# Optimization experiments

Measured on AMD Instinct MI355X. Metric: run time of the kernel, lower is better.

## Reference

```python
import jax, jax.numpy as jnp
import numpy as np


def setup_inputs() -> dict:
    key = jax.random.key(0)
    kx, kw = jax.random.split(key)
    x = jax.random.normal(kx, (4096, 4096), dtype=jnp.float32)
    weight = jax.random.uniform(kw, (7, 7), dtype=jnp.float32)
    bias = jnp.zeros((1,), dtype=jnp.float32)
    return {"x": x, "weight": weight, "bias": bias}


def reference(x, weight, bias):
    # Valid 2D cross-correlation (stride 1, no padding) + scalar bias,
    # identical math to corr2d(X, K) + bias in the torch module.
    lhs = x[None, None, :, :]          # [N=1, C=1, H, W]
    rhs = weight[None, None, :, :]     # [O=1, I=1, kh, kw]
    y = jax.lax.conv_general_dilated(
        lhs, rhs,
        window_strides=(1, 1),
        padding='VALID',
        dimension_numbers=('NCHW', 'OIHW', 'NCHW'),
    )
    return y[0, 0] + bias[0]  # [H-kh+1, W-kw+1]
```

## Files before the change

### kernel.cpp

```cpp
#include <hip/hip_runtime.h>

#define TILE_W 128
#define TILE_H 32
#define HALO   6
#define IN_H   (TILE_H + HALO)
#define LDS_W  136
#define CPR    (LDS_W / 4)
#define TILE_CHUNKS (IN_H * CPR)
#define STAGE_INSTR ((TILE_CHUNKS + 63) / 64)
#define LDS_FLOATS  (STAGE_INSTR * 64 * 4)
#define N  4096
#define ON 4090

__device__ __forceinline__ void gload_lds16(const float* g, float* l) {
    __builtin_amdgcn_global_load_lds(
        (const __attribute__((address_space(1))) void*)g,
        (__attribute__((address_space(3))) void*)l,
        16, 0, 0);
}

__global__ __launch_bounds__(256, 7)
void conv7x7_kernel(const float* __restrict__ x,
                    const float* __restrict__ w,
                    const float* __restrict__ bias,
                    float* __restrict__ out)
{
    __shared__ float tile[LDS_FLOATS];

    const int tid  = threadIdx.x;
    const int lane = tid & 63;
    const int wv   = tid >> 6;
    const int x0   = blockIdx.x * TILE_W;
    const int y0   = blockIdx.y * TILE_H;

    {
        const int xc0 = x0 >> 2;
        for (int k = wv; k < STAGE_INSTR; k += 4) {
            const int m   = (k << 6) + lane;
            const int row = m / CPR;
            const int cc  = m - row * CPR;
            const int gy  = min(y0 + row, N - 1);
            const int gc  = min(xc0 + cc, (N >> 2) - 1);
            const float* src = x + ((size_t)gy << 12) + ((size_t)gc << 2);
            gload_lds16(src, tile + (k << 8));
        }
    }

    float ws[49];
    #pragma unroll
    for (int i = 0; i < 49; ++i) ws[i] = w[i];
    const float bv = bias[0];

    __syncthreads();

    const int tau   = tid & 31;
    const int rg    = tid >> 5;
    const int colf  = tau << 2;
    const int rbase = rg << 2;

    float acc[4][4] = {};

    #pragma unroll
    for (int rr = 0; rr < 10; ++rr) {
        const float* rp = tile + (rbase + rr) * LDS_W + colf;
        float v[10];
        const float4 a = *reinterpret_cast<const float4*>(rp);
        const float4 b = *reinterpret_cast<const float4*>(rp + 4);
        const float2 c = *reinterpret_cast<const float2*>(rp + 8);
        v[0]=a.x; v[1]=a.y; v[2]=a.z; v[3]=a.w;
        v[4]=b.x; v[5]=b.y; v[6]=b.z; v[7]=b.w;
        v[8]=c.x; v[9]=c.y;

        #pragma unroll
        for (int r = 0; r < 4; ++r) {
            const int ky = rr - r;
            if (ky >= 0 && ky < 7) {
                #pragma unroll
                for (int kx = 0; kx < 7; ++kx) {
                    const float wk = ws[ky * 7 + kx];
                    #pragma unroll
                    for (int j = 0; j < 4; ++j)
                        acc[r][j] = fmaf(v[kx + j], wk, acc[r][j]);
                }
            }
        }
    }

    const int ox  = x0 + colf;
    const int oy0 = y0 + rbase;
    if (ox + 4 <= ON && oy0 + 4 <= ON) {
        #pragma unroll
        for (int r = 0; r < 4; ++r) {
            float* dst = out + (size_t)(oy0 + r) * ON + ox;
            *reinterpret_cast<float2*>(dst)     = make_float2(acc[r][0] + bv, acc[r][1] + bv);
            *reinterpret_cast<float2*>(dst + 2) = make_float2(acc[r][2] + bv, acc[r][3] + bv);
        }
    } else {
        #pragma unroll
        for (int r = 0; r < 4; ++r) {
            const int oy = oy0 + r;
            if (oy < ON) {
                float* dst = out + (size_t)oy * ON;
                #pragma unroll
                for (int j = 0; j < 4; ++j) {
                    const int oxj = ox + j;
                    if (oxj < ON) dst[oxj] = acc[r][j] + bv;
                }
            }
        }
    }
}

extern "C" void kernel_launch(void* const* d_in, const int* in_sizes, int n_in,
                              void* d_out, int out_size, void* d_ws, size_t ws_size,
                              hipStream_t stream) {
    const float* x    = (const float*)d_in[0];
    const float* w    = (const float*)d_in[1];
    const float* bias = (const float*)d_in[2];
    float* out        = (float*)d_out;

    dim3 grid((ON + TILE_W - 1) / TILE_W, (ON + TILE_H - 1) / TILE_H);
    conv7x7_kernel<<<grid, dim3(256, 1, 1), 0, stream>>>(x, w, bias, out);
}
```

Before: 35.07 us.

## Give each wave its own 128x8 tile and drop block-wide barrier

Each wavefront now owns an independent 128x8 output tile staged into a private 8 KB LDS buffer. The block barrier is replaced by a per-wave s_waitcnt vmcnt(0), so waves no longer stall on each other. Blocks are remapped through a 1D grid with an XCD-aware swizzle, which lets neighbouring tiles share L2. The cost is more halo reloading, since 14 input rows are loaded for every 8 output rows instead of 38 for 32, so global and L2 traffic goes up.

Result: faster. 33.55 us (-4.3%).

```diff
diff --git a/kernel.cpp b/kernel.cpp
--- a/kernel.cpp
+++ b/kernel.cpp
@@ -1,16 +1,14 @@
 #include <hip/hip_runtime.h>
 
-#define TILE_W 128
-#define TILE_H 32
-#define HALO   6
-#define IN_H   (TILE_H + HALO)
-#define LDS_W  136
-#define CPR    (LDS_W / 4)
-#define TILE_CHUNKS (IN_H * CPR)
-#define STAGE_INSTR ((TILE_CHUNKS + 63) / 64)
-#define LDS_FLOATS  (STAGE_INSTR * 64 * 4)
-#define N  4096
-#define ON 4090
+#define N   4096
+#define ON  4090
+#define LDS_W 136
+#define CPR   34
+#define WBUF  2048
+#define GX  32
+#define GY  512
+#define NT  (GX * GY)
+#define NB  (NT / 4)
 
 __device__ __forceinline__ void gload_lds16(const float* g, float* l) {
     __builtin_amdgcn_global_load_lds(
@@ -19,30 +17,38 @@
         16, 0, 0);
 }
 
-__global__ __launch_bounds__(256, 7)
-void conv7x7_kernel(const float* __restrict__ x,
-                    const float* __restrict__ w,
-                    const float* __restrict__ bias,
-                    float* __restrict__ out)
+__global__ __launch_bounds__(256, 5)
+void conv7x7_wave(const float* __restrict__ x,
+                  const float* __restrict__ w,
+                  const float* __restrict__ bias,
+                  float* __restrict__ out)
 {
-    __shared__ float tile[LDS_FLOATS];
+    __shared__ float lds[4 * WBUF];
 
     const int tid  = threadIdx.x;
     const int lane = tid & 63;
     const int wv   = tid >> 6;
-    const int x0   = blockIdx.x * TILE_W;
-    const int y0   = blockIdx.y * TILE_H;
+    float* buf = lds + (wv << 11);
+
+    const int b  = blockIdx.x;
+    const int bs = (b & 7) * (NB / 8) + (b >> 3);
+    const int t  = (bs << 2) + wv;
+    const int bx = t & (GX - 1);
+    const int by = t >> 5;
+    const int x0 = bx << 7;
+    const int y0 = by << 3;
 
     {
         const int xc0 = x0 >> 2;
-        for (int k = wv; k < STAGE_INSTR; k += 4) {
+        #pragma unroll
+        for (int k = 0; k < 8; ++k) {
             const int m   = (k << 6) + lane;
             const int row = m / CPR;
             const int cc  = m - row * CPR;
             const int gy  = min(y0 + row, N - 1);
             const int gc  = min(xc0 + cc, (N >> 2) - 1);
             const float* src = x + ((size_t)gy << 12) + ((size_t)gc << 2);
-            gload_lds16(src, tile + (k << 8));
+            gload_lds16(src, buf + (k << 8));
         }
     }
 
@@ -51,25 +57,25 @@
     for (int i = 0; i < 49; ++i) ws[i] = w[i];
     const float bv = bias[0];
 
-    __syncthreads();
+    asm volatile("s_waitcnt vmcnt(0)" ::: "memory");
 
-    const int tau   = tid & 31;
-    const int rg    = tid >> 5;
+    const int tau   = lane & 31;
+    const int rg2   = lane >> 5;
     const int colf  = tau << 2;
-    const int rbase = rg << 2;
+    const int rbase = rg2 << 2;
 
     float acc[4][4] = {};
 
     #pragma unroll
     for (int rr = 0; rr < 10; ++rr) {
-        const float* rp = tile + (rbase + rr) * LDS_W + colf;
+        const float* rp = buf + (rbase + rr) * LDS_W + colf;
         float v[10];
         const float4 a = *reinterpret_cast<const float4*>(rp);
-        const float4 b = *reinterpret_cast<const float4*>(rp + 4);
+        const float4 bq = *reinterpret_cast<const float4*>(rp + 4);
         const float2 c = *reinterpret_cast<const float2*>(rp + 8);
-        v[0]=a.x; v[1]=a.y; v[2]=a.z; v[3]=a.w;
-        v[4]=b.x; v[5]=b.y; v[6]=b.z; v[7]=b.w;
-        v[8]=c.x; v[9]=c.y;
+        v[0]=a.x;  v[1]=a.y;  v[2]=a.z;  v[3]=a.w;
+        v[4]=bq.x; v[5]=bq.y; v[6]=bq.z; v[7]=bq.w;
+        v[8]=c.x;  v[9]=c.y;
 
         #pragma unroll
         for (int r = 0; r < 4; ++r) {
@@ -119,6 +125,5 @@
     const float* bias = (const float*)d_in[2];
     float* out        = (float*)d_out;
 
-    dim3 grid((ON + TILE_W - 1) / TILE_W, (ON + TILE_H - 1) / TILE_H);
-    conv7x7_kernel<<<grid, dim3(256, 1, 1), 0, stream>>>(x, w, bias, out);
+    conv7x7_wave<<<dim3(NB, 1, 1), dim3(256, 1, 1), 0, stream>>>(x, w, bias, out);
 }
```
